# Kernel tuning notes

Hardware: AMD Instinct MI355X
Metric: run time of the kernel (lower is better)

Reference implementation:

```python
import jax, jax.numpy as jnp
import numpy as np

N_A = N_B = N_C = 50000
E = 800000
D_IN = 256
D_OUT = 128
T_ATT = 64


def _spmm(row, col, val, ft, n_dst):
    # sparse [n_dst, n_src] @ ft : gather src rows, scale, scatter-add to dst
    return jax.ops.segment_sum(val[:, None] * ft[col], row, num_segments=n_dst)


def setup_inputs() -> dict:
    key = jax.random.key(0)
    ks = jax.random.split(key, 40)
    f32 = jnp.float32
    inp = {
        'x_a': jax.random.normal(ks[0], (N_A, D_IN), f32),
        'x_b': jax.random.normal(ks[1], (N_B, D_IN), f32),
        'x_c': jax.random.normal(ks[2], (N_C, D_IN), f32),
    }
    # COO adjacency per relation: (dst_row, src_col, value)
    rel = {'ab': (N_A, N_B), 'ac': (N_A, N_C), 'ba': (N_B, N_A), 'ca': (N_C, N_A)}
    i = 3
    for name, (nd, ns) in rel.items():
        inp['row_' + name] = jax.random.randint(ks[i], (E,), 0, nd); i += 1
        inp['col_' + name] = jax.random.randint(ks[i], (E,), 0, ns); i += 1
        inp['val_' + name] = jax.random.uniform(ks[i], (E,), f32); i += 1
    # learned parameters (xavier-ish scale)
    def w(k, shape, s=0.05):
        return jax.random.normal(k, shape, f32) * s
    inp['w_self_a'] = w(ks[i], (D_IN, D_OUT)); i += 1
    inp['w_self_b'] = w(ks[i], (D_IN, D_OUT)); i += 1
    inp['w_self_c'] = w(ks[i], (D_IN, D_OUT)); i += 1
    inp['W_ab'] = w(ks[i], (D_IN, D_OUT)); i += 1
    inp['W_ac'] = w(ks[i], (D_IN, D_OUT)); i += 1
    inp['W_ba'] = w(ks[i], (D_IN, D_OUT)); i += 1
    inp['W_ca'] = w(ks[i], (D_IN, D_OUT)); i += 1
    inp['bias_a'] = w(ks[i], (1, D_OUT)); i += 1
    inp['bias_b'] = w(ks[i], (1, D_OUT)); i += 1
    inp['bias_c'] = w(ks[i], (1, D_OUT)); i += 1
    inp['w_cat_a'] = w(ks[i], (2 * D_OUT, D_OUT)); i += 1
    inp['w_cat_b'] = w(ks[i], (2 * D_OUT, D_OUT)); i += 1
    inp['w_cat_c'] = w(ks[i], (2 * D_OUT, D_OUT)); i += 1
    inp['w_query_a'] = w(ks[i], (D_OUT, T_ATT)); i += 1
    inp['w_keys_a'] = w(ks[i], (D_OUT, T_ATT)); i += 1
    inp['w_att_a'] = w(ks[i], (2 * T_ATT, 1)); i += 1
    return inp


def reference(x_a, x_b, x_c,
              row_ab, col_ab, val_ab, row_ac, col_ac, val_ac,
              row_ba, col_ba, val_ba, row_ca, col_ca, val_ca,
              w_self_a, w_self_b, w_self_c,
              W_ab, W_ac, W_ba, W_ca,
              bias_a, bias_b, bias_c,
              w_cat_a, w_cat_b, w_cat_c,
              w_query_a, w_keys_a, w_att_a):
    # ---- type 'a': neighbors [b, c], attention fusion ----
    self_a = x_a @ w_self_a                                   # [Na, D]
    nb_b = _spmm(row_ab, col_ab, val_ab, x_b @ W_ab, N_A)     # [Na, D]
    nb_c = _spmm(row_ac, col_ac, val_ac, x_c @ W_ac, N_A)     # [Na, D]
    q = self_a @ w_query_a                                    # [Na, T]
    e_b = jax.nn.elu(jnp.concatenate([nb_b @ w_keys_a, q], 1) @ w_att_a)  # [Na, 1]
    e_c = jax.nn.elu(jnp.concatenate([nb_c @ w_keys_a, q], 1) @ w_att_a)  # [Na, 1]
    att = jax.nn.softmax(jnp.concatenate([e_b, e_c], 1), axis=1)          # [Na, 2]
    agg_a = nb_b * att[:, :1] + nb_c * att[:, 1:2]
    out_a = jnp.concatenate([agg_a, self_a], 1) @ w_cat_a + bias_a
    # ---- type 'b': single neighbor 'a' ----
    self_b = x_b @ w_self_b
    agg_b = _spmm(row_ba, col_ba, val_ba, x_a @ W_ba, N_B)
    out_b = jnp.concatenate([agg_b, self_b], 1) @ w_cat_b + bias_b
    # ---- type 'c': single neighbor 'a' ----
    self_c = x_c @ w_self_c
    agg_c = _spmm(row_ca, col_ca, val_ca, x_a @ W_ca, N_C)
    out_c = jnp.concatenate([agg_c, self_c], 1) @ w_cat_c + bias_c
    # concat per-type outputs (all D_OUT wide) into one array
    return jnp.concatenate([out_a, out_b, out_c], 0)          # [Na+Nb+Nc, D]
```

## Files before the change

kernel.cpp:

```cpp
#include <hip/hip_runtime.h>

#define NA 50000
#define NE 800000
#define NBKT 196
#define CAP 4608
#define BSTRIDE (NBKT * CAP)

typedef unsigned int   u32;
typedef unsigned short u16;
typedef short s16x8 __attribute__((ext_vector_type(8)));
typedef float f32x4 __attribute__((ext_vector_type(4)));
typedef float f32x2 __attribute__((ext_vector_type(2)));

__device__ __forceinline__ u16 f2bf(float f) {
  u32 u = __float_as_uint(f);
  u += 0x7fffu + ((u >> 16) & 1u);
  return (u16)(u >> 16);
}

__device__ __forceinline__ void accp8(f32x2* a, uint4 q, float v) {
  f32x2 vv; vv[0] = v; vv[1] = v;
  f32x2 f;
  f[0] = __uint_as_float(q.x << 16); f[1] = __uint_as_float(q.x & 0xffff0000u);
  a[0] += vv * f;
  f[0] = __uint_as_float(q.y << 16); f[1] = __uint_as_float(q.y & 0xffff0000u);
  a[1] += vv * f;
  f[0] = __uint_as_float(q.z << 16); f[1] = __uint_as_float(q.z & 0xffff0000u);
  a[2] += vv * f;
  f[0] = __uint_as_float(q.w << 16); f[1] = __uint_as_float(q.w & 0xffff0000u);
  a[3] += vv * f;
}

__device__ __forceinline__ void glds16(const u16* g, u16* l) {
  __builtin_amdgcn_global_load_lds(
      (const __attribute__((address_space(1))) u32*)g,
      (__attribute__((address_space(3))) u32*)l, 16, 0, 0);
}

__device__ __forceinline__ void block_scan256(u32 own, u32* buf, int t) {
  u32 x = own;
  int lane = t & 63;
  #pragma unroll
  for (int off = 1; off < 64; off <<= 1) {
    u32 y = __shfl_up(x, off);
    if (lane >= off) x += y;
  }
  if (lane == 63) buf[t >> 6] = x;
  __syncthreads();
  u32 t0 = buf[0], t1 = buf[1], t2 = buf[2];
  int myw = t >> 6;
  u32 add = (myw > 0 ? t0 : 0u) + (myw > 1 ? t1 : 0u) + (myw > 2 ? t2 : 0u);
  __syncthreads();
  buf[t] = x + add;
  __syncthreads();
}

struct Rel4 { const int* row[4]; const int* col[4]; const float* val[4]; };

struct Prep {
  const float* src[10]; u16* dst[10];
  const float* wq; const float* wk; const float* wa; float* uvp;
};

struct ConvArgs { const float* x[3]; u16* xb; };

struct FtArgs { const u16* A[3]; const u16* Bt[3]; u16* C[3]; };

struct FuseW { const u16* Wf[3]; const float* bias[3]; float* out[3]; };

__global__ __launch_bounds__(256) void k_main1(Rel4 R, u32* __restrict__ gcur,
                                               uint2* __restrict__ pairs, ConvArgs CA,
                                               Prep P) {
  __shared__ __align__(16) char smem[40960];
  const int gy = blockIdx.y;
  const int t = threadIdx.x;
  if (gy < 4) {
    if (blockIdx.x >= 196) return;
    int rel = gy;
    int e0 = blockIdx.x * 4096;
    int nrem = min(4096, NE - e0);
    u32* sw0  = (u32*)smem;
    u32* sval = sw0 + 4096;
    unsigned char* sbkt = (unsigned char*)(sval + 4096);
    u32* hist  = (u32*)(sbkt + 4096);
    u32* lscan = hist + 256;
    u32* cnt2  = lscan + 256;
    u32* gbase = cnt2 + 256;
    hist[t] = 0; cnt2[t] = 0;
    __syncthreads();
    const int* rr = R.row[rel];
    const int* cc = R.col[rel];
    const float* vl = R.val[rel];
    u32 w0[16]; u32 vv[16]; int bb[16];
    #pragma unroll
    for (int i = 0; i < 16; ++i) {
      int li = t + i * 256;
      bool ok = li < nrem;
      int idx = e0 + (ok ? li : 0);
      int r = ok ? rr[idx] : 0;
      int c = ok ? cc[idx] : 0;
      float v = ok ? vl[idx] : 0.f;
      u32 b = (u32)r >> 8;
      w0[i] = (u32)(c & 0xFFFF) | ((u32)(r & 255) << 16) | (b << 24);
      vv[i] = __float_as_uint(v);
      bb[i] = ok ? (int)b : -1;
      if (ok) atomicAdd(&hist[b], 1u);
    }
    __syncthreads();
    u32 own = hist[t];
    block_scan256(own, lscan, t);
    gbase[t] = (u32)t * CAP + atomicAdd(&gcur[rel * 256 + t], own);
    #pragma unroll
    for (int i = 0; i < 16; ++i) {
      if (bb[i] >= 0) {
        int b = bb[i];
        u32 p = (lscan[b] - hist[b]) + atomicAdd(&cnt2[b], 1u);
        sw0[p] = w0[i]; sval[p] = vv[i]; sbkt[p] = (unsigned char)b;
      }
    }
    __syncthreads();
    uint2* Pp = pairs + (size_t)rel * BSTRIDE;
    #pragma unroll
    for (int i = 0; i < 16; ++i) {
      int p = t + i * 256;
      if (p < nrem) {
        int b = sbkt[p];
        u32 gd = gbase[b] + (u32)p - (lscan[b] - hist[b]);
        uint2 pr; pr.x = sw0[p]; pr.y = sval[p];
        Pp[gd] = pr;
      }
    }
  } else if (gy < 11) {
    const size_t TOT = 38400000;
    const size_t TSZ = 12800000;
    size_t base = ((size_t)(gy - 4) * 391 + blockIdx.x) * 16384 + (size_t)t * 8;
    #pragma unroll
    for (int it = 0; it < 8; ++it) {
      size_t g = base + (size_t)it * 2048;
      if (g < TOT) {
        int which = (g >= 2 * TSZ) ? 2 : (g >= TSZ ? 1 : 0);
        size_t off = g - (size_t)which * TSZ;
        const float* sp = CA.x[which] + off;
        float4 v0 = *(const float4*)(sp);
        float4 v1 = *(const float4*)(sp + 4);
        s16x8 o;
        o[0] = (short)f2bf(v0.x); o[1] = (short)f2bf(v0.y);
        o[2] = (short)f2bf(v0.z); o[3] = (short)f2bf(v0.w);
        o[4] = (short)f2bf(v1.x); o[5] = (short)f2bf(v1.y);
        o[6] = (short)f2bf(v1.z); o[7] = (short)f2bf(v1.w);
        *(s16x8*)(CA.xb + g) = o;
      }
    }
  } else {
    const int bx = blockIdx.x;
    if (bx < 320) {
      #pragma unroll
      for (int rep = 0; rep < 4; ++rep) {
        int idx = bx * 1024 + rep * 256 + t;
        int w = idx >> 15;
        int r = idx & 32767;
        if (w < 7) {
          int k = r & 255, n = r >> 8;
          P.dst[w][n * 256 + k] = f2bf(P.src[w][k * 128 + n]);
        } else {
          int e = r & 7, l = (r >> 3) & 63, jj = (r >> 9) & 7, ks = r >> 12;
          int n = jj * 16 + (l & 15);
          int k = ks * 32 + ((l >> 4) * 8) + e;
          P.dst[w][r] = f2bf(P.src[w][k * 128 + n]);
        }
      }
    } else if (bx == 320) {
      int d = t & 127, which = t >> 7;
      const float* w = which ? P.wq : P.wk;
      const float* a = P.wa + which * 64;
      float s = 0.f;
      for (int i = 0; i < 64; ++i) s += w[d * 64 + i] * a[i];
      P.uvp[which * 128 + d] = s;
    }
  }
}

__global__ __launch_bounds__(256) void k_main2(const u32* __restrict__ gcur,
    int* __restrict__ ofs_s, int* __restrict__ ofs_e,
    const uint2* __restrict__ pairs, u32* __restrict__ epak, FtArgs Ar) {
  __shared__ __align__(16) char smem[40960];
  const int gy = blockIdx.y;
  const int t = threadIdx.x;
  if (gy < 4) {
    if (blockIdx.x >= 196) return;
    int rel = gy;
    int b = blockIdx.x;
    int base = b * CAP;
    int n = (int)gcur[rel * 256 + b];
    u32* sw0  = (u32*)smem;
    u32* sv   = sw0 + CAP;
    u32* hist = sv + CAP;
    u32* scan = hist + 256;
    u32* cur  = scan + 256;
    hist[t] = 0;
    __syncthreads();
    const uint2* P = pairs + (size_t)rel * BSTRIDE;
    for (int p = t; p < n; p += 256) {
      uint2 pr = P[base + p];
      sw0[p] = pr.x; sv[p] = pr.y;
      atomicAdd(&hist[(pr.x >> 16) & 255], 1u);
    }
    __syncthreads();
    u32 own = hist[t];
    block_scan256(own, scan, t);
    u32 excl = scan[t] - own;
    cur[t] = excl;
    int r0 = b << 8;
    if (r0 + t < NA) {
      ofs_s[(size_t)rel * NA + r0 + t] = base + (int)excl;
      ofs_e[(size_t)rel * NA + r0 + t] = base + (int)(excl + own);
    }
    __syncthreads();
    u32* E = epak + (size_t)rel * BSTRIDE;
    for (int p = t; p < n; p += 256) {
      u32 w = sw0[p];
      int rl = (w >> 16) & 255;
      u32 d = atomicAdd(&cur[rl], 1u);
      E[base + (int)d] = (w & 0xFFFFu) | ((u32)f2bf(__uint_as_float(sv[p])) << 16);
    }
  } else {
    u16* Asl = (u16*)smem;
    u16* Bsl = Asl + 128 * 64;
    const int by = gy - 4;
    const int which = (by < 3) ? 0 : (by < 5 ? 1 : 2);
    const int col0 = (by - (which == 0 ? 0 : (which == 1 ? 3 : 5))) * 128;
    const int ldc = (which == 0) ? 384 : 256;
    const u16* A = Ar.A[which];
    const u16* Bt = Ar.Bt[which] + (size_t)col0 * 256;
    u16* C = Ar.C[which] + col0;
    const int row0 = blockIdx.x * 128;
    const int w = t >> 6, l = t & 63;
    const int wr = (w >> 1) * 64, wc = (w & 1) * 64;
    f32x4 acc[4][4] = {};
    for (int kk = 0; kk < 4; ++kk) {
      #pragma unroll
      for (int q = 0; q < 4; ++q) {
        int c = q * 256 + t;
        int r = c >> 3, col8 = (c & 7) * 8;
        int gr = row0 + r; gr = gr < NA ? gr : NA - 1;
        glds16(A + (size_t)gr * 256 + kk * 64 + col8, Asl + c * 8);
        glds16(Bt + (size_t)r * 256 + kk * 64 + col8, Bsl + c * 8);
      }
      __syncthreads();
      #pragma unroll
      for (int ks = 0; ks < 2; ++ks) {
        s16x8 af[4], bfr[4];
        #pragma unroll
        for (int i = 0; i < 4; ++i)
          af[i] = *(const s16x8*)&Asl[(wr + i * 16 + (l & 15)) * 64 + ks * 32 + (l >> 4) * 8];
        #pragma unroll
        for (int j = 0; j < 4; ++j)
          bfr[j] = *(const s16x8*)&Bsl[(wc + j * 16 + (l & 15)) * 64 + ks * 32 + (l >> 4) * 8];
        #pragma unroll
        for (int i = 0; i < 4; ++i)
          #pragma unroll
          for (int j = 0; j < 4; ++j)
            acc[i][j] = __builtin_amdgcn_mfma_f32_16x16x32_bf16(af[i], bfr[j], acc[i][j], 0, 0, 0);
      }
      __syncthreads();
    }
    #pragma unroll
    for (int i = 0; i < 4; ++i)
      #pragma unroll
      for (int j = 0; j < 4; ++j)
        #pragma unroll
        for (int q = 0; q < 4; ++q) {
          int r = row0 + wr + i * 16 + (l >> 4) * 4 + q;
          if (r < NA) C[(size_t)r * ldc + wc + j * 16 + (l & 15)] = f2bf(acc[i][j][q]);
        }
  }
}

__global__ __launch_bounds__(256) void k_spmm(
    const int* __restrict__ ofs_s, const int* __restrict__ ofs_e,
    const u32* __restrict__ epak,
    const u16* __restrict__ ya, const u16* __restrict__ yb, const u16* __restrict__ yc,
    const float* __restrict__ uv, FuseW FW) {
  __shared__ u16 Asm[16 * 264];
  int tid = threadIdx.x;
  int lane = tid & 63, wid = tid >> 6;
  int g = lane >> 4, gl = lane & 15;
  const u32 glb = (u32)gl * 16;
  int lr = wid * 4 + g;
  int row = blockIdx.x * 16 + lr;
  int gy = blockIdx.y;
  if (gy == 0) {
    const char* ybase = (const char*)yb;
    const char* cbase = (const char*)yc;
    f32x2 fb2[4] = {}; f32x2 fc2[4] = {};
    {
      int i = ofs_s[row], e = ofs_e[row];
      for (; i + 4 <= e; i += 4) {
        u32 p0 = epak[i], p1 = epak[i + 1], p2 = epak[i + 2], p3 = epak[i + 3];
        uint4 q0 = *(const uint4*)(ybase + (((p0 & 0xFFFFu) << 9) + glb));
        uint4 q1 = *(const uint4*)(ybase + (((p1 & 0xFFFFu) << 9) + glb));
        uint4 q2 = *(const uint4*)(ybase + (((p2 & 0xFFFFu) << 9) + glb));
        uint4 q3 = *(const uint4*)(ybase + (((p3 & 0xFFFFu) << 9) + glb));
        accp8(fb2, q0, __uint_as_float(p0 & 0xffff0000u));
        accp8(fb2, q1, __uint_as_float(p1 & 0xffff0000u));
        accp8(fb2, q2, __uint_as_float(p2 & 0xffff0000u));
        accp8(fb2, q3, __uint_as_float(p3 & 0xffff0000u));
      }
      for (; i < e; ++i) {
        u32 p0 = epak[i];
        uint4 q0 = *(const uint4*)(ybase + (((p0 & 0xFFFFu) << 9) + glb));
        accp8(fb2, q0, __uint_as_float(p0 & 0xffff0000u));
      }
    }
    {
      const u32* pr = epak + BSTRIDE;
      int i = ofs_s[NA + row], e = ofs_e[NA + row];
      for (; i + 4 <= e; i += 4) {
        u32 p0 = pr[i], p1 = pr[i + 1], p2 = pr[i + 2], p3 = pr[i + 3];
        uint4 q0 = *(const uint4*)(cbase + (((p0 & 0xFFFFu) << 9) + glb));
        uint4 q1 = *(const uint4*)(cbase + (((p1 & 0xFFFFu) << 9) + glb));
        uint4 q2 = *(const uint4*)(cbase + (((p2 & 0xFFFFu) << 9) + glb));
        uint4 q3 = *(const uint4*)(cbase + (((p3 & 0xFFFFu) << 9) + glb));
        accp8(fc2, q0, __uint_as_float(p0 & 0xffff0000u));
        accp8(fc2, q1, __uint_as_float(p1 & 0xffff0000u));
        accp8(fc2, q2, __uint_as_float(p2 & 0xffff0000u));
        accp8(fc2, q3, __uint_as_float(p3 & 0xffff0000u));
      }
      for (; i < e; ++i) {
        u32 p0 = pr[i];
        uint4 q0 = *(const uint4*)(cbase + (((p0 & 0xFFFFu) << 9) + glb));
        accp8(fc2, q0, __uint_as_float(p0 & 0xffff0000u));
      }
    }
    float fb[8], fc[8];
    #pragma unroll
    for (int j = 0; j < 8; ++j) { fb[j] = fb2[j >> 1][j & 1]; fc[j] = fc2[j >> 1][j & 1]; }
    uint4 sq = *(const uint4*)((const char*)ya + (u32)row * 768 + glb);
    float sf[8];
    sf[0] = __uint_as_float(sq.x << 16); sf[1] = __uint_as_float(sq.x & 0xffff0000u);
    sf[2] = __uint_as_float(sq.y << 16); sf[3] = __uint_as_float(sq.y & 0xffff0000u);
    sf[4] = __uint_as_float(sq.z << 16); sf[5] = __uint_as_float(sq.z & 0xffff0000u);
    sf[6] = __uint_as_float(sq.w << 16); sf[7] = __uint_as_float(sq.w & 0xffff0000u);
    float pb = 0.f, pc = 0.f, pq = 0.f;
    const float* up = uv + gl * 8;
    const float* vp = uv + 128 + gl * 8;
    #pragma unroll
    for (int j = 0; j < 8; ++j) {
      pb += fb[j] * up[j];
      pc += fc[j] * up[j];
      pq += sf[j] * vp[j];
    }
    #pragma unroll
    for (int off = 1; off < 16; off <<= 1) {
      pb += __shfl_xor(pb, off);
      pc += __shfl_xor(pc, off);
      pq += __shfl_xor(pq, off);
    }
    float eb = pb + pq, ec = pc + pq;
    eb = eb > 0.f ? eb : (expf(eb) - 1.f);
    ec = ec > 0.f ? ec : (expf(ec) - 1.f);
    float m = fmaxf(eb, ec);
    float p0 = expf(eb - m), p1 = expf(ec - m);
    float inv = 1.f / (p0 + p1);
    float a0 = p0 * inv, a1 = p1 * inv;
    s16x8 av;
    #pragma unroll
    for (int j = 0; j < 8; ++j) av[j] = (short)f2bf(a0 * fb[j] + a1 * fc[j]);
    *(s16x8*)&Asm[lr * 264 + gl * 8] = av;
    *(s16x8*)&Asm[lr * 264 + 128 + gl * 8] = *(s16x8*)&sq;
  } else {
    const int which = gy - 1;
    const int* os = ofs_s + (2 + which) * NA;
    const int* oe = ofs_e + (2 + which) * NA;
    const u32* pr = epak + (size_t)(2 + which) * BSTRIDE;
    const char* fbase = (const char*)ya + (which ? 512 : 256);
    const char* selfp = (const char*)(which ? yc : yb);
    f32x2 fa2[4] = {};
    int i = os[row], e = oe[row];
    for (; i + 4 <= e; i += 4) {
      u32 p0 = pr[i], p1 = pr[i + 1], p2 = pr[i + 2], p3 = pr[i + 3];
      uint4 q0 = *(const uint4*)(fbase + ((p0 & 0xFFFFu) * 768u + glb));
      uint4 q1 = *(const uint4*)(fbase + ((p1 & 0xFFFFu) * 768u + glb));
      uint4 q2 = *(const uint4*)(fbase + ((p2 & 0xFFFFu) * 768u + glb));
      uint4 q3 = *(const uint4*)(fbase + ((p3 & 0xFFFFu) * 768u + glb));
      accp8(fa2, q0, __uint_as_float(p0 & 0xffff0000u));
      accp8(fa2, q1, __uint_as_float(p1 & 0xffff0000u));
      accp8(fa2, q2, __uint_as_float(p2 & 0xffff0000u));
      accp8(fa2, q3, __uint_as_float(p3 & 0xffff0000u));
    }
    for (; i < e; ++i) {
      u32 p0 = pr[i];
      uint4 q0 = *(const uint4*)(fbase + ((p0 & 0xFFFFu) * 768u + glb));
      accp8(fa2, q0, __uint_as_float(p0 & 0xffff0000u));
    }
    s16x8 av;
    #pragma unroll
    for (int j = 0; j < 8; ++j) av[j] = (short)f2bf(fa2[j >> 1][j & 1]);
    *(s16x8*)&Asm[lr * 264 + gl * 8] = av;
    *(s16x8*)&Asm[lr * 264 + 128 + gl * 8] =
        *(const s16x8*)(selfp + (u32)row * 512 + 256 + glb);
  }
  __syncthreads();
  const u16* Wf = FW.Wf[gy];
  const float* bias = FW.bias[gy];
  float* outp = FW.out[gy];
  const int j0 = wid * 2, j1 = wid * 2 + 1;
  f32x4 acc0 = {0.f, 0.f, 0.f, 0.f}, acc1 = {0.f, 0.f, 0.f, 0.f};
  #pragma unroll
  for (int ks = 0; ks < 8; ++ks) {
    s16x8 a = *(const s16x8*)&Asm[(lane & 15) * 264 + ks * 32 + (lane >> 4) * 8];
    s16x8 b0 = *(const s16x8*)(Wf + ((size_t)(ks * 8 + j0) * 64 + lane) * 8);
    s16x8 b1 = *(const s16x8*)(Wf + ((size_t)(ks * 8 + j1) * 64 + lane) * 8);
    acc0 = __builtin_amdgcn_mfma_f32_16x16x32_bf16(a, b0, acc0, 0, 0, 0);
    acc1 = __builtin_amdgcn_mfma_f32_16x16x32_bf16(a, b1, acc1, 0, 0, 0);
  }
  const int c0 = j0 * 16 + (lane & 15), c1 = j1 * 16 + (lane & 15);
  const float b0v = bias[c0], b1v = bias[c1];
  const int rbase = blockIdx.x * 16 + (lane >> 4) * 4;
  #pragma unroll
  for (int q = 0; q < 4; ++q) {
    __builtin_nontemporal_store(acc0[q] + b0v, &outp[(size_t)(rbase + q) * 128 + c0]);
    __builtin_nontemporal_store(acc1[q] + b1v, &outp[(size_t)(rbase + q) * 128 + c1]);
  }
}

extern "C" void kernel_launch(void* const* d_in, const int* in_sizes, int n_in,
                              void* d_out, int out_size, void* d_ws, size_t ws_size,
                              hipStream_t stream) {
  const float* x_a = (const float*)d_in[0];
  const float* x_b = (const float*)d_in[1];
  const float* x_c = (const float*)d_in[2];
  const int* row_ab = (const int*)d_in[3];
  const int* col_ab = (const int*)d_in[4];
  const float* val_ab = (const float*)d_in[5];
  const int* row_ac = (const int*)d_in[6];
  const int* col_ac = (const int*)d_in[7];
  const float* val_ac = (const float*)d_in[8];
  const int* row_ba = (const int*)d_in[9];
  const int* col_ba = (const int*)d_in[10];
  const float* val_ba = (const float*)d_in[11];
  const int* row_ca = (const int*)d_in[12];
  const int* col_ca = (const int*)d_in[13];
  const float* val_ca = (const float*)d_in[14];
  const float* w_self_a = (const float*)d_in[15];
  const float* w_self_b = (const float*)d_in[16];
  const float* w_self_c = (const float*)d_in[17];
  const float* W_ab = (const float*)d_in[18];
  const float* W_ac = (const float*)d_in[19];
  const float* W_ba = (const float*)d_in[20];
  const float* W_ca = (const float*)d_in[21];
  const float* bias_a = (const float*)d_in[22];
  const float* bias_b = (const float*)d_in[23];
  const float* bias_c = (const float*)d_in[24];
  const float* w_cat_a = (const float*)d_in[25];
  const float* w_cat_b = (const float*)d_in[26];
  const float* w_cat_c = (const float*)d_in[27];
  const float* w_query_a = (const float*)d_in[28];
  const float* w_keys_a = (const float*)d_in[29];
  const float* w_att_a = (const float*)d_in[30];

  float* out = (float*)d_out;

  char* ws = (char*)d_ws;
  size_t off_b = 0;
  auto walloc = [&](size_t bytes) {
    void* p = ws + off_b;
    off_b = (off_b + bytes + 255) & ~(size_t)255;
    return p;
  };
  u16* ya = (u16*)walloc((size_t)NA * 384 * 2);
  u16* yb = (u16*)walloc((size_t)NA * 256 * 2);
  u16* yc = (u16*)walloc((size_t)NA * 256 * 2);
  int* ofs_s = (int*)walloc((size_t)4 * NA * 4);
  int* ofs_e = (int*)walloc((size_t)4 * NA * 4);
  u32* gcur = (u32*)walloc((size_t)4 * 256 * 4);
  uint2* pairs = (uint2*)walloc((size_t)4 * BSTRIDE * 8);
  u32* epak = (u32*)walloc((size_t)4 * BSTRIDE * 4);
  u16* Wa_t = (u16*)walloc((size_t)384 * 256 * 2);
  u16* Wb_t = (u16*)walloc((size_t)256 * 256 * 2);
  u16* Wc_t = (u16*)walloc((size_t)256 * 256 * 2);
  u16* Wcat_a = (u16*)walloc((size_t)128 * 256 * 2);
  u16* Wcat_b = (u16*)walloc((size_t)128 * 256 * 2);
  u16* Wcat_c = (u16*)walloc((size_t)128 * 256 * 2);
  float* uvbuf = (float*)walloc(256 * 4);
  u16* xb = (u16*)walloc((size_t)3 * NA * 256 * 2);

  Rel4 R;
  R.row[0] = row_ab; R.col[0] = col_ab; R.val[0] = val_ab;
  R.row[1] = row_ac; R.col[1] = col_ac; R.val[1] = val_ac;
  R.row[2] = row_ba; R.col[2] = col_ba; R.val[2] = val_ba;
  R.row[3] = row_ca; R.col[3] = col_ca; R.val[3] = val_ca;

  Prep P;
  P.src[0] = w_self_a; P.dst[0] = Wa_t;
  P.src[1] = W_ba;     P.dst[1] = Wa_t + 128 * 256;
  P.src[2] = W_ca;     P.dst[2] = Wa_t + 256 * 256;
  P.src[3] = W_ab;     P.dst[3] = Wb_t;
  P.src[4] = w_self_b; P.dst[4] = Wb_t + 128 * 256;
  P.src[5] = W_ac;     P.dst[5] = Wc_t;
  P.src[6] = w_self_c; P.dst[6] = Wc_t + 128 * 256;
  P.src[7] = w_cat_a;  P.dst[7] = Wcat_a;
  P.src[8] = w_cat_b;  P.dst[8] = Wcat_b;
  P.src[9] = w_cat_c;  P.dst[9] = Wcat_c;
  P.wq = w_query_a; P.wk = w_keys_a; P.wa = w_att_a; P.uvp = uvbuf;

  hipMemsetAsync(gcur, 0, (size_t)4 * 256 * 4, stream);

  ConvArgs CA;
  CA.x[0] = x_a; CA.x[1] = x_b; CA.x[2] = x_c;
  CA.xb = xb;
  dim3 g1(391, 12);
  k_main1<<<g1, 256, 0, stream>>>(R, gcur, pairs, CA, P);

  FtArgs FA;
  FA.A[0] = xb; FA.A[1] = xb + (size_t)NA * 256; FA.A[2] = xb + (size_t)2 * NA * 256;
  FA.Bt[0] = Wa_t; FA.Bt[1] = Wb_t; FA.Bt[2] = Wc_t;
  FA.C[0] = ya; FA.C[1] = yb; FA.C[2] = yc;
  dim3 g2(391, 11);
  k_main2<<<g2, 256, 0, stream>>>(gcur, ofs_s, ofs_e, pairs, epak, FA);

  FuseW FW;
  FW.Wf[0] = Wcat_a; FW.Wf[1] = Wcat_b; FW.Wf[2] = Wcat_c;
  FW.bias[0] = bias_a; FW.bias[1] = bias_b; FW.bias[2] = bias_c;
  FW.out[0] = out; FW.out[1] = out + (size_t)NA * 128; FW.out[2] = out + (size_t)NA * 128 * 2;
  dim3 gs(3125, 3);
  k_spmm<<<gs, 256, 0, stream>>>(ofs_s, ofs_e, epak, ya, yb, yc, uvbuf, FW);
}
```

Before: 259.7 us.

## Fuse fp32-to-bf16 input conversion into the feature GEMM tile load

Drops the separate pass that converted x_a/x_b/x_c to a bf16 buffer in k_main1. The GEMM in k_main2 now reads fp32 rows directly, converts them to bf16 in registers, and writes them to a padded LDS tile (row stride 72) for the A operand. This removes the 77MB bf16 intermediate write and its re-read, and shrinks the first launch grid. In exchange each x row is read as fp32 several times, once per column-tile block (3 for a, 2 for b and c), and the A load now goes through synchronous register conversion instead of direct global-to-LDS copies.

Measured after the change: 262.6 us. About the same (+1.1%).

```diff
diff --git a/kernel.cpp b/kernel.cpp
--- a/kernel.cpp
+++ b/kernel.cpp
@@ -62,15 +62,12 @@
   const float* wq; const float* wk; const float* wa; float* uvp;
 };
 
-struct ConvArgs { const float* x[3]; u16* xb; };
-
-struct FtArgs { const u16* A[3]; const u16* Bt[3]; u16* C[3]; };
+struct FtArgs { const float* A[3]; const u16* Bt[3]; u16* C[3]; };
 
 struct FuseW { const u16* Wf[3]; const float* bias[3]; float* out[3]; };
 
 __global__ __launch_bounds__(256) void k_main1(Rel4 R, u32* __restrict__ gcur,
-                                               uint2* __restrict__ pairs, ConvArgs CA,
-                                               Prep P) {
+                                               uint2* __restrict__ pairs, Prep P) {
   __shared__ __align__(16) char smem[40960];
   const int gy = blockIdx.y;
   const int t = threadIdx.x;
@@ -128,27 +125,6 @@
         u32 gd = gbase[b] + (u32)p - (lscan[b] - hist[b]);
         uint2 pr; pr.x = sw0[p]; pr.y = sval[p];
         Pp[gd] = pr;
-      }
-    }
-  } else if (gy < 11) {
-    const size_t TOT = 38400000;
-    const size_t TSZ = 12800000;
-    size_t base = ((size_t)(gy - 4) * 391 + blockIdx.x) * 16384 + (size_t)t * 8;
-    #pragma unroll
-    for (int it = 0; it < 8; ++it) {
-      size_t g = base + (size_t)it * 2048;
-      if (g < TOT) {
-        int which = (g >= 2 * TSZ) ? 2 : (g >= TSZ ? 1 : 0);
-        size_t off = g - (size_t)which * TSZ;
-        const float* sp = CA.x[which] + off;
-        float4 v0 = *(const float4*)(sp);
-        float4 v1 = *(const float4*)(sp + 4);
-        s16x8 o;
-        o[0] = (short)f2bf(v0.x); o[1] = (short)f2bf(v0.y);
-        o[2] = (short)f2bf(v0.z); o[3] = (short)f2bf(v0.w);
-        o[4] = (short)f2bf(v1.x); o[5] = (short)f2bf(v1.y);
-        o[6] = (short)f2bf(v1.z); o[7] = (short)f2bf(v1.w);
-        *(s16x8*)(CA.xb + g) = o;
       }
     }
   } else {
@@ -224,27 +200,47 @@
       E[base + (int)d] = (w & 0xFFFFu) | ((u32)f2bf(__uint_as_float(sv[p])) << 16);
     }
   } else {
-    u16* Asl = (u16*)smem;
-    u16* Bsl = Asl + 128 * 64;
+    u16* Al = (u16*)smem;
+    u16* Bl = Al + 128 * 72;
     const int by = gy - 4;
     const int which = (by < 3) ? 0 : (by < 5 ? 1 : 2);
     const int col0 = (by - (which == 0 ? 0 : (which == 1 ? 3 : 5))) * 128;
     const int ldc = (which == 0) ? 384 : 256;
-    const u16* A = Ar.A[which];
+    const float* A = Ar.A[which];
     const u16* Bt = Ar.Bt[which] + (size_t)col0 * 256;
     u16* C = Ar.C[which] + col0;
     const int row0 = blockIdx.x * 128;
     const int w = t >> 6, l = t & 63;
     const int wr = (w >> 1) * 64, wc = (w & 1) * 64;
+    const int sr = t >> 1, kb = (t & 1) * 32;
     f32x4 acc[4][4] = {};
     for (int kk = 0; kk < 4; ++kk) {
       #pragma unroll
       for (int q = 0; q < 4; ++q) {
         int c = q * 256 + t;
         int r = c >> 3, col8 = (c & 7) * 8;
-        int gr = row0 + r; gr = gr < NA ? gr : NA - 1;
-        glds16(A + (size_t)gr * 256 + kk * 64 + col8, Asl + c * 8);
-        glds16(Bt + (size_t)r * 256 + kk * 64 + col8, Bsl + c * 8);
+        glds16(Bt + (size_t)r * 256 + kk * 64 + col8, Bl + c * 8);
+      }
+      if (row0 + sr < NA) {
+        const float* ap = A + (size_t)(row0 + sr) * 256 + kk * 64 + kb;
+        #pragma unroll
+        for (int h = 0; h < 2; ++h) {
+          float f[16];
+          #pragma unroll
+          for (int i = 0; i < 4; ++i) {
+            float4 v4 = *(const float4*)(ap + h * 16 + i * 4);
+            f[4*i] = v4.x; f[4*i+1] = v4.y; f[4*i+2] = v4.z; f[4*i+3] = v4.w;
+          }
+          s16x8 v0, v1;
+          #pragma unroll
+          for (int i = 0; i < 8; ++i) { v0[i] = (short)f2bf(f[i]); v1[i] = (short)f2bf(f[i + 8]); }
+          *(s16x8*)&Al[sr * 72 + kb + h * 16]     = v0;
+          *(s16x8*)&Al[sr * 72 + kb + h * 16 + 8] = v1;
+        }
+      } else {
+        s16x8 z = {0,0,0,0,0,0,0,0};
+        #pragma unroll
+        for (int h = 0; h < 4; ++h) *(s16x8*)&Al[sr * 72 + kb + h * 8] = z;
       }
       __syncthreads();
       #pragma unroll
@@ -252,10 +248,10 @@
         s16x8 af[4], bfr[4];
         #pragma unroll
         for (int i = 0; i < 4; ++i)
-          af[i] = *(const s16x8*)&Asl[(wr + i * 16 + (l & 15)) * 64 + ks * 32 + (l >> 4) * 8];
+          af[i] = *(const s16x8*)&Al[(wr + i * 16 + (l & 15)) * 72 + ks * 32 + (l >> 4) * 8];
         #pragma unroll
         for (int j = 0; j < 4; ++j)
-          bfr[j] = *(const s16x8*)&Bsl[(wc + j * 16 + (l & 15)) * 64 + ks * 32 + (l >> 4) * 8];
+          bfr[j] = *(const s16x8*)&Bl[(wc + j * 16 + (l & 15)) * 64 + ks * 32 + (l >> 4) * 8];
         #pragma unroll
         for (int i = 0; i < 4; ++i)
           #pragma unroll
@@ -483,7 +479,6 @@
   u16* Wcat_b = (u16*)walloc((size_t)128 * 256 * 2);
   u16* Wcat_c = (u16*)walloc((size_t)128 * 256 * 2);
   float* uvbuf = (float*)walloc(256 * 4);
-  u16* xb = (u16*)walloc((size_t)3 * NA * 256 * 2);
 
   Rel4 R;
   R.row[0] = row_ab; R.col[0] = col_ab; R.val[0] = val_ab;
@@ -506,14 +501,11 @@
 
   hipMemsetAsync(gcur, 0, (size_t)4 * 256 * 4, stream);
 
-  ConvArgs CA;
-  CA.x[0] = x_a; CA.x[1] = x_b; CA.x[2] = x_c;
-  CA.xb = xb;
-  dim3 g1(391, 12);
-  k_main1<<<g1, 256, 0, stream>>>(R, gcur, pairs, CA, P);
+  dim3 g1(321, 5);
+  k_main1<<<g1, 256, 0, stream>>>(R, gcur, pairs, P);
 
   FtArgs FA;
-  FA.A[0] = xb; FA.A[1] = xb + (size_t)NA * 256; FA.A[2] = xb + (size_t)2 * NA * 256;
+  FA.A[0] = x_a; FA.A[1] = x_b; FA.A[2] = x_c;
   FA.Bt[0] = Wa_t; FA.Bt[1] = Wb_t; FA.Bt[2] = Wc_t;
   FA.C[0] = ya; FA.C[1] = yb; FA.C[2] = yc;
   dim3 g2(391, 11);
```
